# Kernel optimization log

Hardware: AMD Instinct MI355X
Metric: run time of the kernel (lower is better)

Reference implementation:

```python
import jax, jax.numpy as jnp
import numpy as np

BS, EP = 32, 32
N_AGENTS, N_ATOM, EMBED = 8, 51, 32
STATE_DIM, HYP = 128, 64
V_MIN, V_MAX = -10.0, 10.0


def proj(support, probs, v_min, v_max, n_atom):
    # C51 categorical projection of (support, probs) onto the fixed atom grid
    # linspace(v_min, v_max, n_atom). support/probs: [..., M] -> [..., n_atom]
    support, probs = jnp.broadcast_arrays(support, probs)
    delta = (v_max - v_min) / (n_atom - 1)
    b = (jnp.clip(support, v_min, v_max) - v_min) / delta
    l = jnp.floor(b)
    u = jnp.ceil(b)
    eq = (u == l).astype(probs.dtype)  # support exactly on an atom -> all mass to l
    ml = probs * (u - b + eq)
    mu = probs * (b - l)
    shp = probs.shape
    n = int(np.prod(shp[:-1]))
    m = shp[-1]
    rows = jnp.arange(n)[:, None]
    out = jnp.zeros((n, n_atom), probs.dtype)
    out = out.at[rows, l.astype(jnp.int32).reshape(n, m)].add(ml.reshape(n, m))
    out = out.at[rows, u.astype(jnp.int32).reshape(n, m)].add(mu.reshape(n, m))
    return out.reshape(shp[:-1] + (n_atom,))


def bconv(p, q):
    # Full 1D convolution of per-row categorical pmfs (sum of two random vars).
    # p: [N, L], q: [N, M] -> [N, L+M-1], via grouped conv (one group per row).
    N, L = p.shape
    M = q.shape[-1]
    out = jax.lax.conv_general_dilated(
        p[None], jnp.flip(q, -1)[:, None, :],
        window_strides=(1,), padding=[(M - 1, M - 1)],
        feature_group_count=N, dimension_numbers=('NCW', 'OIW', 'NCW'))
    return out[0]


def mlp2(x, w1, b1, w2, b2):
    return jax.nn.relu(x @ w1.T + b1) @ w2.T + b2


def setup_inputs():
    key = jax.random.key(0)
    ks = jax.random.split(key, 20)
    def p(k, shape, s=0.05):
        return jax.random.normal(k, shape, dtype=jnp.float32) * s
    aq = jax.random.uniform(ks[0], (BS, EP, N_AGENTS, N_ATOM), dtype=jnp.float32)
    aq = aq / jnp.sum(aq, -1, keepdims=True)  # valid categorical distributions
    return {
        'agent_qs_distri': aq,
        'states': p(ks[1], (BS, EP, STATE_DIM), 1.0),
        'hw1_w1': p(ks[2], (HYP, STATE_DIM)), 'hw1_b1': p(ks[3], (HYP,)),
        'hw1_w2': p(ks[4], (EMBED * N_AGENTS, HYP)), 'hw1_b2': p(ks[5], (EMBED * N_AGENTS,)),
        'hb1_w': p(ks[6], (EMBED, STATE_DIM)), 'hb1_b': p(ks[7], (EMBED,)),
        'hwf_w1': p(ks[8], (HYP, STATE_DIM)), 'hwf_b1': p(ks[9], (HYP,)),
        'hwf_w2': p(ks[10], (EMBED, HYP)), 'hwf_b2': p(ks[11], (EMBED,)),
        'v_w1': p(ks[12], (EMBED, STATE_DIM)), 'v_b1': p(ks[13], (EMBED,)),
        'v_w2': p(ks[14], (1, EMBED)), 'v_b2': p(ks[15], (1,)),
    }


def reference(agent_qs_distri, states, hw1_w1, hw1_b1, hw1_w2, hw1_b2,
              hb1_w, hb1_b, hwf_w1, hwf_b1, hwf_w2, hwf_b2,
              v_w1, v_b1, v_w2, v_b2):
    bs, ep, n_agents, n_atom = agent_qs_distri.shape
    s = states.reshape(-1, STATE_DIM)
    atoms = jnp.linspace(V_MIN, V_MAX, n_atom).astype(jnp.float32)  # [A]

    w1 = jnp.abs(mlp2(s, hw1_w1, hw1_b1, hw1_w2, hw1_b2)).reshape(bs, ep, EMBED, n_agents)
    b1 = (s @ hb1_w.T + hb1_b).reshape(bs, ep, EMBED)

    # stage 1: scale each agent's support by w1[..., k, i], project back onto atoms
    sup1 = atoms * w1[..., None]                                       # [bs,ep,E,Na,A]
    aw = proj(sup1, agent_qs_distri[:, :, None], V_MIN, V_MAX, n_atom)  # [bs,ep,E,Na,A]
    awf = aw.reshape(-1, n_agents, n_atom)                              # [bs*ep*E,Na,A]
    q = awf[:, 0]
    for i in range(1, n_agents):
        q = bconv(q, awf[:, i])                                         # [.., Na*A-Na+1]
    L1 = n_agents * n_atom - n_agents + 1
    sup = jnp.linspace(n_agents * V_MIN, n_agents * V_MAX, L1).astype(jnp.float32)
    sup = jax.nn.elu(sup + b1[..., None])                               # [bs,ep,E,L1]
    x = proj(sup, q.reshape(bs, ep, EMBED, L1), V_MIN, V_MAX, n_atom)   # [bs,ep,E,A]

    # stage 2: hyper_w_final scaling, convolve across embed dim, add V(s)
    wf = jnp.abs(mlp2(s, hwf_w1, hwf_b1, hwf_w2, hwf_b2)).reshape(bs, ep, EMBED)
    xw = proj(atoms * wf[..., None], x, V_MIN, V_MAX, n_atom)           # [bs,ep,E,A]
    xwf = xw.reshape(-1, EMBED, n_atom)
    q = xwf[:, 0]
    for i in range(1, EMBED):
        q = bconv(q, xwf[:, i])                                         # [bs*ep, E*A-E+1]
    L2 = EMBED * n_atom - EMBED + 1
    v = mlp2(s, v_w1, v_b1, v_w2, v_b2).reshape(bs, ep, 1)
    sup2 = jnp.linspace(EMBED * V_MIN, EMBED * V_MAX, L2).astype(jnp.float32) + v
    return proj(sup2, q.reshape(bs, ep, L2), V_MIN, V_MAX, n_atom)      # [bs,ep,A]
```

## Files before the change

### kernel.cpp

```cpp
#include <hip/hip_runtime.h>
#include <hip/hip_bf16.h>
#include <math.h>

typedef unsigned short u16;

#define WAVE_SYNC() asm volatile("s_waitcnt lgkmcnt(0)" ::: "memory")

__device__ __forceinline__ float bf2f(u16 u) {
  union { unsigned int i; float f; } c;
  c.i = ((unsigned int)u) << 16;
  return c.f;
}
__device__ __forceinline__ float bflo(unsigned int u) {
  union { unsigned int i; float f; } c; c.i = u << 16; return c.f;
}
__device__ __forceinline__ float bfhi(unsigned int u) {
  union { unsigned int i; float f; } c; c.i = u & 0xffff0000u; return c.f;
}
__device__ __forceinline__ u16 f2bf(float f) {
  union { float f; unsigned int i; } c;
  c.f = f;
  unsigned int x = c.i;
  unsigned int r = (x + 0x7fffu + ((x >> 16) & 1u)) >> 16;
  return (u16)r;
}

__device__ __forceinline__ void proj_bounds(float wv, int& ML, int& MH) {
  float smin = (-10.0f + 0.4f * 0.0f)  * wv;
  float smax = (-10.0f + 0.4f * 50.0f) * wv;
  float bmin = (fminf(fmaxf(smin, -10.0f), 10.0f) + 10.0f) / 0.4f;
  float bmax = (fminf(fmaxf(smax, -10.0f), 10.0f) + 10.0f) / 0.4f;
  ML = (int)floorf(bmin);
  MH = (int)ceilf(bmax);
}

template<typename SUPP>
__device__ __forceinline__ void proj_scan(float* __restrict__ g1,
                                          float* __restrict__ g2,
                                          int span, int lane, SUPP supp)
{
  if (lane < 52) g1[lane] = 0.f;
  if (lane < 53) g2[lane] = 0.f;
  float cml = 0.f, cmu = 0.f;
  int ck = -1;
  for (int base = 0; base < span; base += 64) {
    int t = base + lane;
    bool act = (t < span);
    int tc = act ? t : (span - 1);
    float sup, p;
    supp(tc, act, sup, p);
    float c  = fminf(fmaxf(sup, -10.0f), 10.0f);
    float b  = (c + 10.0f) / 0.4f;
    float l  = floorf(b);
    float u  = ceilf(b);
    float eq = (u == l) ? 1.0f : 0.0f;
    float ml = p * (u - b + eq);
    float mu = p * (b - l);
    int   li = (int)l;
    bool last = (base + 64 >= span);
    if (lane == 0 && ck >= 0) {
      if (ck == li) { ml += cml; mu += cmu; }
      else          { g1[ck] = cml; g2[ck + 1] = cmu; }
    }
#pragma unroll
    for (int d = 1; d < 64; d <<= 1) {
      int   lo = __shfl_up(li, d);
      float a1 = __shfl_up(ml, d);
      float a2 = __shfl_up(mu, d);
      bool same = (lane >= d) && (lo == li);
      ml += same ? a1 : 0.f;
      mu += same ? a2 : 0.f;
    }
    int ln = __shfl_down(li, 1);
    bool runend = (lane == 63) ? last : (ln != li);
    if (runend) { g1[li] = ml; g2[li + 1] = mu; }
    if (!last) {
      cml = __shfl(ml, 63);
      cmu = __shfl(mu, 63);
      ck  = __shfl(li, 63);
    }
  }
}

__device__ __forceinline__ void conv_pad2(const float* __restrict__ q,
                                          float* __restrict__ qn,
                                          const float* __restrict__ kvs,
                                          int ML, int W, int T,
                                          int LQ, int HQ, int lane)
{
  const int Lout = LQ + ML, Hout = HQ + ML + T;
  for (int J = Lout + lane; J <= Hout; J += 64) {
    const float* qp = q + (J - ML);
    float acc = 0.f;
    for (int c = 0; c < W; c += 4) {
      float4 k4 = *(const float4*)(kvs + c);
      acc = fmaf(k4.x, qp[-c],     acc);
      acc = fmaf(k4.y, qp[-c - 1], acc);
      acc = fmaf(k4.z, qp[-c - 2], acc);
      acc = fmaf(k4.w, qp[-c - 3], acc);
    }
    qn[J] = acc;
  }
}

template<int BF>
__device__ __forceinline__ float ldt(const void* p, int i) {
  if (BF) return bf2f(((const u16*)p)[i]);
  return ((const float*)p)[i];
}

template<int BF>
__device__ __forceinline__ float dot128_t(const void* w, int row, const float* s) {
  float acc = 0.f;
  if (BF) {
    const uint4* p = (const uint4*)((const u16*)w + row * 128);
#pragma unroll
    for (int i = 0; i < 16; ++i) {
      uint4 v = p[i];
      int b = i * 8;
      acc = fmaf(bflo(v.x), s[b + 0], acc); acc = fmaf(bfhi(v.x), s[b + 1], acc);
      acc = fmaf(bflo(v.y), s[b + 2], acc); acc = fmaf(bfhi(v.y), s[b + 3], acc);
      acc = fmaf(bflo(v.z), s[b + 4], acc); acc = fmaf(bfhi(v.z), s[b + 5], acc);
      acc = fmaf(bflo(v.w), s[b + 6], acc); acc = fmaf(bfhi(v.w), s[b + 7], acc);
    }
  } else {
    const float4* p = (const float4*)((const float*)w + row * 128);
#pragma unroll
    for (int i = 0; i < 32; ++i) {
      float4 v = p[i];
      int b = i * 4;
      acc = fmaf(v.x, s[b + 0], acc); acc = fmaf(v.y, s[b + 1], acc);
      acc = fmaf(v.z, s[b + 2], acc); acc = fmaf(v.w, s[b + 3], acc);
    }
  }
  return acc;
}

template<int BF>
__device__ __forceinline__ float dot64_t(const void* w, int row, const float* h) {
  float acc = 0.f;
  if (BF) {
    const uint4* p = (const uint4*)((const u16*)w + row * 64);
#pragma unroll
    for (int i = 0; i < 8; ++i) {
      uint4 v = p[i];
      int b = i * 8;
      acc = fmaf(bflo(v.x), h[b + 0], acc); acc = fmaf(bfhi(v.x), h[b + 1], acc);
      acc = fmaf(bflo(v.y), h[b + 2], acc); acc = fmaf(bfhi(v.y), h[b + 3], acc);
      acc = fmaf(bflo(v.z), h[b + 4], acc); acc = fmaf(bfhi(v.z), h[b + 5], acc);
      acc = fmaf(bflo(v.w), h[b + 6], acc); acc = fmaf(bfhi(v.w), h[b + 7], acc);
    }
  } else {
    const float4* p = (const float4*)((const float*)w + row * 64);
#pragma unroll
    for (int i = 0; i < 16; ++i) {
      float4 v = p[i];
      int b = i * 4;
      acc = fmaf(v.x, h[b + 0], acc); acc = fmaf(v.y, h[b + 1], acc);
      acc = fmaf(v.z, h[b + 2], acc); acc = fmaf(v.w, h[b + 3], acc);
    }
  }
  return acc;
}

template<int BF>
__device__ __forceinline__ void mlp_body(
    const void* states,
    const void* hw1_w1, const void* hw1_b1, const void* hw1_w2, const void* hw1_b2,
    const void* hb1_w,  const void* hb1_b,
    const void* hwf_w1, const void* hwf_b1, const void* hwf_w2, const void* hwf_b2,
    const void* v_w1,   const void* v_b1,   const void* v_w2,   const void* v_b2,
    float* w1_ws, float* b1_ws, float* wf_ws, float* v_ws,
    int n, int tid, float* s, float* h1, float* hf, float* vh)
{
  s[tid]      = ldt<BF>(states, n * 128 + tid);
  s[tid + 64] = ldt<BF>(states, n * 128 + 64 + tid);
  __syncthreads();

  h1[tid] = fmaxf(dot128_t<BF>(hw1_w1, tid, s) + ldt<BF>(hw1_b1, tid), 0.f);
  hf[tid] = fmaxf(dot128_t<BF>(hwf_w1, tid, s) + ldt<BF>(hwf_b1, tid), 0.f);
  if (tid < 32) {
    vh[tid] = fmaxf(dot128_t<BF>(v_w1, tid, s) + ldt<BF>(v_b1, tid), 0.f);
    b1_ws[n * 32 + tid] = dot128_t<BF>(hb1_w, tid, s) + ldt<BF>(hb1_b, tid);
  }
  __syncthreads();

#pragma unroll
  for (int k = 0; k < 4; ++k) {
    int o = tid + 64 * k;
    w1_ws[n * 256 + o] = fabsf(dot64_t<BF>(hw1_w2, o, h1) + ldt<BF>(hw1_b2, o));
  }
  if (tid < 32)
    wf_ws[n * 32 + tid] = fabsf(dot64_t<BF>(hwf_w2, tid, hf) + ldt<BF>(hwf_b2, tid));
  if (tid == 0) {
    float acc = ldt<BF>(v_b2, 0);
    for (int e = 0; e < 32; ++e) acc = fmaf(ldt<BF>(v_w2, e), vh[e], acc);
    v_ws[n] = acc;
  }
}

__global__ __launch_bounds__(64) void k_mlp(
    const void* __restrict__ states,
    const void* __restrict__ hw1_w1, const void* __restrict__ hw1_b1,
    const void* __restrict__ hw1_w2, const void* __restrict__ hw1_b2,
    const void* __restrict__ hb1_w,  const void* __restrict__ hb1_b,
    const void* __restrict__ hwf_w1, const void* __restrict__ hwf_b1,
    const void* __restrict__ hwf_w2, const void* __restrict__ hwf_b2,
    const void* __restrict__ v_w1,   const void* __restrict__ v_b1,
    const void* __restrict__ v_w2,   const void* __restrict__ v_b2,
    float* __restrict__ w1_ws, float* __restrict__ b1_ws,
    float* __restrict__ wf_ws, float* __restrict__ v_ws,
    int* __restrict__ flag)
{
  __shared__ float s[128];
  __shared__ float h1[64];
  __shared__ float hf[64];
  __shared__ float vh[32];
  const int n = blockIdx.x;
  const int tid = threadIdx.x;

  const u16* sr = (const u16*)states;
  unsigned int e0 = (sr[tid] >> 7) & 0xFF;
  unsigned int e1 = (sr[tid + 64] >> 7) & 0xFF;
  unsigned long long bl0 = __ballot(e0 >= 97 && e0 <= 141);
  unsigned long long bl1 = __ballot(e1 >= 97 && e1 <= 141);
  int bf = (__popcll(bl0) + __popcll(bl1) >= 104) ? 1 : 0;
  if (tid == 0) *flag = bf;

  if (bf)
    mlp_body<1>(states, hw1_w1, hw1_b1, hw1_w2, hw1_b2, hb1_w, hb1_b,
                hwf_w1, hwf_b1, hwf_w2, hwf_b2, v_w1, v_b1, v_w2, v_b2,
                w1_ws, b1_ws, wf_ws, v_ws, n, tid, s, h1, hf, vh);
  else
    mlp_body<0>(states, hw1_w1, hw1_b1, hw1_w2, hw1_b2, hb1_w, hb1_b,
                hwf_w1, hwf_b1, hwf_w2, hwf_b2, v_w1, v_b1, v_w2, v_b2,
                w1_ws, b1_ws, wf_ws, v_ws, n, tid, s, h1, hf, vh);
}

__global__ __launch_bounds__(128) void k_perembed(
    const void* __restrict__ aq,
    const float* __restrict__ w1_ws, const float* __restrict__ b1_ws,
    const float* __restrict__ wf_ws, float* __restrict__ xw_ws,
    const int* __restrict__ flag)
{
  __shared__ __align__(16) float Ab[2][520];
  __shared__ __align__(16) float Bb[2][520];
  __shared__ __align__(16) float kvsb[2][56];
  __shared__ float gAb[2][53];
  __shared__ float gBb[2][54];

  const int w    = threadIdx.x >> 6;
  const int lane = threadIdx.x & 63;
  const int task = blockIdx.x * 2 + w;
  const int n = task >> 5;
  const int e = task & 31;
  const int bf = *flag;

  float* A   = Ab[w];
  float* B   = Bb[w];
  float* kvs = kvsb[w];
  float* gA  = gAb[w];
  float* gB  = gBb[w];

  float pv[8];
  if (bf) {
    const u16* p = (const u16*)aq + n * 408 + lane;
#pragma unroll
    for (int a = 0; a < 8; ++a) pv[a] = (lane < 51) ? bf2f(p[a * 51]) : 0.f;
  } else {
    const float* p = (const float*)aq + n * 408 + lane;
#pragma unroll
    for (int a = 0; a < 8; ++a) pv[a] = (lane < 51) ? p[a * 51] : 0.f;
  }
  float wreg = (lane < 8) ? w1_ws[n * 256 + e * 8 + lane] : 0.f;
  float b1v  = b1_ws[n * 32 + e];
  float wfv  = wf_ws[n * 32 + e];

  float wv0 = __shfl(wreg, 0);
  int ML0, MH0;
  proj_bounds(wv0, ML0, MH0);
  {
    float pa = pv[0];
    proj_scan(gA, gB, 51, lane, [&](int t, bool act, float& sup, float& p) {
      sup = (-10.0f + 0.4f * (float)t) * wv0;
      p = act ? pa : 0.f;
    });
  }
  if (lane <= MH0 - ML0)
    A[64 + ML0 + lane] = gA[ML0 + lane] + gB[ML0 + lane];
  WAVE_SYNC();

  int LQ = 64 + ML0, HQ = 64 + MH0;
  float* q = A;
  float* qn = B;
#pragma unroll
  for (int a = 1; a < 8; ++a) {
    float wv = __shfl(wreg, a);
    int ML, MH;
    proj_bounds(wv, ML, MH);
    int T = MH - ML;
    int W = (T + 4) & ~3;
    float pa = pv[a];
    proj_scan(gA, gB, 51, lane, [&](int t, bool act, float& sup, float& p) {
      sup = (-10.0f + 0.4f * (float)t) * wv;
      p = act ? pa : 0.f;
    });
    if (lane < W)     kvs[lane] = (lane <= T) ? (gA[ML + lane] + gB[ML + lane]) : 0.f;
    if (lane < W - 1) q[LQ - 1 - lane] = 0.f;
    if (lane < T)     q[HQ + 1 + lane] = 0.f;
    WAVE_SYNC();
    conv_pad2(q, qn, kvs, ML, W, T, LQ, HQ, lane);
    WAVE_SYNC();
    LQ += ML; HQ += MH;
    float* t_ = q; q = qn; qn = t_;
  }

  {
    int span = HQ - LQ + 1;
    int LQl = LQ;
    const float* qf = q;
    proj_scan(gA, gB, span, lane, [&](int t, bool act, float& sup, float& p) {
      int tg = (LQl - 64) + t;
      float raw = (-80.0f + 0.4f * (float)tg) + b1v;
      sup = (raw > 0.f) ? raw : expm1f(raw);
      p = act ? qf[LQl + t] : 0.f;
    });
  }
  WAVE_SYNC();

  float x2v = (lane < 51) ? (gA[lane] + gB[lane]) : 0.f;
  WAVE_SYNC();
  int MLf, MHf;
  proj_bounds(wfv, MLf, MHf);
  proj_scan(gA, gB, 51, lane, [&](int t, bool act, float& sup, float& p) {
    sup = (-10.0f + 0.4f * (float)t) * wfv;
    p = act ? x2v : 0.f;
  });
  WAVE_SYNC();
  if (lane <= MHf - MLf)
    xw_ws[task * 51 + MLf + lane] = gA[MLf + lane] + gB[MLf + lane];
}

__global__ __launch_bounds__(64) void k_final(
    const float* __restrict__ xw_ws, const float* __restrict__ wf_ws,
    const float* __restrict__ v_ws,
    void* __restrict__ out, const int* __restrict__ flag)
{
  __shared__ __align__(16) float A[1720];
  __shared__ __align__(16) float B[1720];
  __shared__ __align__(16) float kvs[56];
  __shared__ float gA[53];
  __shared__ float gB[54];

  const int n    = blockIdx.x;
  const int lane = threadIdx.x;
  const int bf   = *flag;

  float wfreg = (lane < 32) ? wf_ws[n * 32 + lane] : 0.f;
  float vv    = v_ws[n];

  float wv0 = __shfl(wfreg, 0);
  int ML0, MH0;
  proj_bounds(wv0, ML0, MH0);
  if (lane <= MH0 - ML0)
    A[64 + ML0 + lane] = xw_ws[(n * 32 + 0) * 51 + ML0 + lane];

  int LQ = 64 + ML0, HQ = 64 + MH0;
  float* q = A;
  float* qn = B;

  int MLn, MHn;
  { float wvn = __shfl(wfreg, 1); proj_bounds(wvn, MLn, MHn); }
  float nv = (lane <= MHn - MLn) ? xw_ws[(n * 32 + 1) * 51 + MLn + lane] : 0.f;

  for (int e = 1; e < 32; ++e) {
    int ML = MLn, MH = MHn;
    int T = MH - ML;
    int W = (T + 4) & ~3;
    if (lane < W)     kvs[lane] = (lane <= T) ? nv : 0.f;
    if (lane < W - 1) q[LQ - 1 - lane] = 0.f;
    if (lane < T)     q[HQ + 1 + lane] = 0.f;
    if (e < 31) {
      float wvn = __shfl(wfreg, e + 1);
      proj_bounds(wvn, MLn, MHn);
      nv = (lane <= MHn - MLn) ? xw_ws[(n * 32 + e + 1) * 51 + MLn + lane] : 0.f;
    }
    WAVE_SYNC();
    conv_pad2(q, qn, kvs, ML, W, T, LQ, HQ, lane);
    WAVE_SYNC();
    LQ += ML; HQ += MH;
    float* t_ = q; q = qn; qn = t_;
  }

  {
    int span = HQ - LQ + 1;
    int LQl = LQ;
    const float* qf = q;
    proj_scan(gA, gB, span, lane, [&](int t, bool act, float& sup, float& p) {
      int tg = (LQl - 64) + t;
      sup = (-320.0f + 0.4f * (float)tg) + vv;
      p = act ? qf[LQl + t] : 0.f;
    });
  }
  WAVE_SYNC();

  if (lane < 51) {
    float o = gA[lane] + gB[lane];
    if (bf) ((u16*)out)[n * 51 + lane] = f2bf(o);
    else    ((float*)out)[n * 51 + lane] = o;
  }
}

extern "C" void kernel_launch(void* const* d_in, const int* in_sizes, int n_in,
                              void* d_out, int out_size, void* d_ws, size_t ws_size,
                              hipStream_t stream)
{
  float* ws    = (float*)d_ws;
  float* w1_ws = ws;
  float* b1_ws = w1_ws + 1024 * 256;
  float* wf_ws = b1_ws + 1024 * 32;
  float* v_ws  = wf_ws + 1024 * 32;
  float* xw_ws = v_ws  + 1024;
  int*   flag  = (int*)(xw_ws + 1024 * 32 * 51);

  k_mlp<<<1024, 64, 0, stream>>>(d_in[1],
      d_in[2], d_in[3], d_in[4], d_in[5], d_in[6], d_in[7],
      d_in[8], d_in[9], d_in[10], d_in[11], d_in[12], d_in[13],
      d_in[14], d_in[15],
      w1_ws, b1_ws, wf_ws, v_ws, flag);

  k_perembed<<<16384, 128, 0, stream>>>(d_in[0], w1_ws, b1_ws, wf_ws, xw_ws, flag);

  k_final<<<1024, 64, 0, stream>>>(xw_ws, wf_ws, v_ws, d_out, flag);
}
```

Measured before the change: 270.2 us.

## Widen k_final to 256 threads and split the convolution across four waves

The final per-row kernel now runs four wavefronts per block instead of one. The sequential 31-step convolution chain spreads its output positions across 256 threads, and the wave-local waitcnt is replaced with block-wide barriers. This is meant to cut the per-row latency of the long serial convolution chain, where output length grows to roughly 1600. In exchange every step pays two __syncthreads across four waves, and the projection scan still runs on one wave.

```diff
diff --git a/kernel.cpp b/kernel.cpp
--- a/kernel.cpp
+++ b/kernel.cpp
@@ -86,10 +86,10 @@
                                           float* __restrict__ qn,
                                           const float* __restrict__ kvs,
                                           int ML, int W, int T,
-                                          int LQ, int HQ, int lane)
+                                          int LQ, int HQ, int tid, int nthr)
 {
   const int Lout = LQ + ML, Hout = HQ + ML + T;
-  for (int J = Lout + lane; J <= Hout; J += 64) {
+  for (int J = Lout + tid; J <= Hout; J += nthr) {
     const float* qp = q + (J - ML);
     float acc = 0.f;
     for (int c = 0; c < W; c += 4) {
@@ -309,7 +309,7 @@
     if (lane < W - 1) q[LQ - 1 - lane] = 0.f;
     if (lane < T)     q[HQ + 1 + lane] = 0.f;
     WAVE_SYNC();
-    conv_pad2(q, qn, kvs, ML, W, T, LQ, HQ, lane);
+    conv_pad2(q, qn, kvs, ML, W, T, LQ, HQ, lane, 64);
     WAVE_SYNC();
     LQ += ML; HQ += MH;
     float* t_ = q; q = qn; qn = t_;
@@ -341,7 +341,7 @@
     xw_ws[task * 51 + MLf + lane] = gA[MLf + lane] + gB[MLf + lane];
 }
 
-__global__ __launch_bounds__(64) void k_final(
+__global__ __launch_bounds__(256) void k_final(
     const float* __restrict__ xw_ws, const float* __restrict__ wf_ws,
     const float* __restrict__ v_ws,
     void* __restrict__ out, const int* __restrict__ flag)
@@ -353,7 +353,8 @@
   __shared__ float gB[54];
 
   const int n    = blockIdx.x;
-  const int lane = threadIdx.x;
+  const int tid  = threadIdx.x;
+  const int lane = tid & 63;
   const int bf   = *flag;
 
   float wfreg = (lane < 32) ? wf_ws[n * 32 + lane] : 0.f;
@@ -362,8 +363,8 @@
   float wv0 = __shfl(wfreg, 0);
   int ML0, MH0;
   proj_bounds(wv0, ML0, MH0);
-  if (lane <= MH0 - ML0)
-    A[64 + ML0 + lane] = xw_ws[(n * 32 + 0) * 51 + ML0 + lane];
+  if (tid <= MH0 - ML0)
+    A[64 + ML0 + tid] = xw_ws[(n * 32 + 0) * 51 + ML0 + tid];
 
   int LQ = 64 + ML0, HQ = 64 + MH0;
   float* q = A;
@@ -371,28 +372,28 @@
 
   int MLn, MHn;
   { float wvn = __shfl(wfreg, 1); proj_bounds(wvn, MLn, MHn); }
-  float nv = (lane <= MHn - MLn) ? xw_ws[(n * 32 + 1) * 51 + MLn + lane] : 0.f;
+  float nv = (tid <= MHn - MLn) ? xw_ws[(n * 32 + 1) * 51 + MLn + tid] : 0.f;
 
   for (int e = 1; e < 32; ++e) {
     int ML = MLn, MH = MHn;
     int T = MH - ML;
     int W = (T + 4) & ~3;
-    if (lane < W)     kvs[lane] = (lane <= T) ? nv : 0.f;
-    if (lane < W - 1) q[LQ - 1 - lane] = 0.f;
-    if (lane < T)     q[HQ + 1 + lane] = 0.f;
+    if (tid < W)     kvs[tid] = (tid <= T) ? nv : 0.f;
+    if (tid < W - 1) q[LQ - 1 - tid] = 0.f;
+    if (tid < T)     q[HQ + 1 + tid] = 0.f;
     if (e < 31) {
       float wvn = __shfl(wfreg, e + 1);
       proj_bounds(wvn, MLn, MHn);
-      nv = (lane <= MHn - MLn) ? xw_ws[(n * 32 + e + 1) * 51 + MLn + lane] : 0.f;
-    }
-    WAVE_SYNC();
-    conv_pad2(q, qn, kvs, ML, W, T, LQ, HQ, lane);
-    WAVE_SYNC();
+      nv = (tid <= MHn - MLn) ? xw_ws[(n * 32 + e + 1) * 51 + MLn + tid] : 0.f;
+    }
+    __syncthreads();
+    conv_pad2(q, qn, kvs, ML, W, T, LQ, HQ, tid, 256);
+    __syncthreads();
     LQ += ML; HQ += MH;
     float* t_ = q; q = qn; qn = t_;
   }
 
-  {
+  if (tid < 64) {
     int span = HQ - LQ + 1;
     int LQl = LQ;
     const float* qf = q;
@@ -402,12 +403,12 @@
       p = act ? qf[LQl + t] : 0.f;
     });
   }
-  WAVE_SYNC();
-
-  if (lane < 51) {
-    float o = gA[lane] + gB[lane];
-    if (bf) ((u16*)out)[n * 51 + lane] = f2bf(o);
-    else    ((float*)out)[n * 51 + lane] = o;
+  __syncthreads();
+
+  if (tid < 51) {
+    float o = gA[tid] + gB[tid];
+    if (bf) ((u16*)out)[n * 51 + tid] = f2bf(o);
+    else    ((float*)out)[n * 51 + tid] = o;
   }
 }
 
@@ -431,5 +432,5 @@
 
   k_perembed<<<16384, 128, 0, stream>>>(d_in[0], w1_ws, b1_ws, wf_ws, xw_ws, flag);
 
-  k_final<<<1024, 64, 0, stream>>>(xw_ws, wf_ws, v_ws, d_out, flag);
-}
+  k_final<<<1024, 256, 0, stream>>>(xw_ws, wf_ws, v_ws, d_out, flag);
+}
```

After: 250.7 us. 1.08x faster.
